# Kernel optimization log

Measured on AMD Instinct MI355X. Metric: run time of the kernel, lower is better.

The kernel has to match this reference:

```python
import jax, jax.numpy as jnp
import numpy as np

# Loihi neuron constants (from a typical slayerSNN network.yaml)
I_DECAY = 1024.0   # current decay (of 4096)
V_DECAY = 128.0    # voltage decay (of 4096)
THETA = 100.0      # firing threshold


def spike_loihi(x):
    """Loihi CUBA neuron dynamics over trailing time axis. x: [..., T] weighted input."""
    xT = jnp.moveaxis(x, -1, 0)  # [T, ...]
    a_i = (4096.0 - I_DECAY) / 4096.0
    a_v = (4096.0 - V_DECAY) / 4096.0

    def step(carry, xt):
        u, v = carry
        u = a_i * u + xt           # synaptic current
        v = a_v * v + u            # membrane voltage
        s = (v >= THETA).astype(x.dtype)
        v = v * (1.0 - s)          # reset on spike
        return (u, v), s

    z = jnp.zeros(xT.shape[1:], x.dtype)
    _, s = jax.lax.scan(step, (z, z), xT)
    return jnp.moveaxis(s, 0, -1)


def delay_shift(x):
    """Shift spikes by 1 timestep along last axis (slayer.delayShift(spike, 1))."""
    return jnp.concatenate([jnp.zeros_like(x[..., :1]), x[..., :-1]], axis=-1)


def conv_t(x, w):
    """Per-timestep 2D conv, padding 1. x: [N,C,H,W,T], w: [O,I,3,3]."""
    N, C, H, W, T = x.shape
    xt = jnp.transpose(x, (0, 4, 1, 2, 3)).reshape(N * T, C, H, W)
    y = jax.lax.conv_general_dilated(xt, w, (1, 1), [(1, 1), (1, 1)],
                                     dimension_numbers=('NCHW', 'OIHW', 'NCHW'))
    O = w.shape[0]
    return jnp.transpose(y.reshape(N, T, O, H, W), (0, 2, 3, 4, 1))


def sum_pool2(x, w):
    """slayer.pool(2): 2x2 sum-pool scaled by (loaded) scalar pool weight."""
    N, C, H, W, T = x.shape
    return x.reshape(N, C, H // 2, 2, W // 2, 2, T).sum(axis=(3, 5)) * w


def setup_inputs() -> dict:
    key = jax.random.key(0)
    ks = jax.random.split(key, 8)
    N, T = 16, 128
    spike = jax.random.bernoulli(ks[0], 0.1, (N, 2, 40, 40, T)).astype(jnp.float32)
    conv1_w = jax.random.normal(ks[1], (8, 2, 3, 3), jnp.float32) * 0.5
    conv2_w = jax.random.normal(ks[2], (16, 8, 3, 3), jnp.float32) * 0.05
    conv3_w = jax.random.normal(ks[3], (32, 16, 3, 3), jnp.float32) * 0.05
    fc1_w = jax.random.normal(ks[4], (512, 10 * 10 * 32), jnp.float32) * 0.02
    pool1_w = jnp.asarray(1.1, jnp.float32)
    pool2_w = jnp.asarray(1.1, jnp.float32)
    return {"spike": spike, "conv1_w": conv1_w, "conv2_w": conv2_w,
            "conv3_w": conv3_w, "pool1_w": pool1_w, "pool2_w": pool2_w,
            "fc1_w": fc1_w}


def reference(spike, conv1_w, conv2_w, conv3_w, pool1_w, pool2_w, fc1_w):
    x = spike_loihi(conv_t(spike, conv1_w * 20.0))    # weightScale=20
    x = delay_shift(x)
    x = spike_loihi(sum_pool2(x, pool1_w))
    x = delay_shift(x)
    x = spike_loihi(conv_t(x, conv2_w * 100.0))       # weightScale=100
    x = delay_shift(x)
    x = spike_loihi(sum_pool2(x, pool2_w))
    x = delay_shift(x)
    x = spike_loihi(conv_t(x, conv3_w * 100.0))       # weightScale=100
    N, T = x.shape[0], x.shape[-1]
    x = x.reshape(N, -1, 1, 1, T)                     # [N, 3200, 1, 1, T]
    x = delay_shift(x)
    x = spike_loihi(jnp.einsum('nchwt,oc->nohwt', x, fc1_w))
    x = delay_shift(x)
    return x
```

## Files before the change

kernel.cpp:

```cpp
#include <hip/hip_runtime.h>
#include <stdint.h>


#define T 128
#define AI 0.75f
#define AV 0.96875f
#define THETA 100.0f

typedef __attribute__((ext_vector_type(8))) short v8s;
typedef __attribute__((ext_vector_type(16))) float v16f;

__device__ __forceinline__ void neuron_step(float x, float& u, float& v, float& s) {
    u = AI * u + x;
    v = AV * v + u;
    s = (v >= THETA) ? 1.0f : 0.0f;
    v = v * (1.0f - s);
}

__global__ __launch_bounds__(256) void conv1_scan(
    const float* __restrict__ in, const float* __restrict__ cw,
    uint8_t* __restrict__ sout)
{
    __shared__ float ldsF[64 * 130];
    int bid = blockIdx.x;
    int wg = bid % 5;
    int hy = (bid / 5) % 40;
    int n  = bid / 200;
    int tid = threadIdx.x;
    int wxl = tid >> 5, tt = tid & 31, t0 = tt * 4;
    int wx = wg * 8 + wxl;

    float4 tap[18];
    #pragma unroll
    for (int c = 0; c < 2; c++)
      #pragma unroll
      for (int dh = 0; dh < 3; dh++)
        #pragma unroll
        for (int dw = 0; dw < 3; dw++) {
            int q = c * 9 + dh * 3 + dw;
            int hh = hy + dh - 1, ww = wx + dw - 1;
            bool ok = (hh >= 0) && (hh < 40) && (ww >= 0) && (ww < 40);
            tap[q] = ok ? *(const float4*)(in +
                (((size_t)(n * 2 + c) * 40 + hh) * 40 + ww) * T + t0)
                        : make_float4(0.f, 0.f, 0.f, 0.f);
        }

    #pragma unroll
    for (int o = 0; o < 8; o++) {
        const float* wp = cw + o * 18;
        float a0 = 0.f, a1 = 0.f, a2 = 0.f, a3 = 0.f;
        #pragma unroll
        for (int q = 0; q < 18; q++) {
            a0 += wp[q] * tap[q].x;  a1 += wp[q] * tap[q].y;
            a2 += wp[q] * tap[q].z;  a3 += wp[q] * tap[q].w;
        }
        float* xr = &ldsF[(o * 8 + wxl) * 130 + t0];
        xr[0] = a0 * 20.0f; xr[1] = a1 * 20.0f;
        xr[2] = a2 * 20.0f; xr[3] = a3 * 20.0f;
    }
    __syncthreads();
    if (tid < 64) {
        int o = tid >> 3, wxl2 = tid & 7;
        float u = 0.f, v = 0.f;
        uint32_t ob[32];
        const float* xr = &ldsF[tid * 130];
        #pragma unroll
        for (int tb = 0; tb < 32; tb++) {
            float s0, s1, s2, s3;
            neuron_step(xr[tb * 4 + 0], u, v, s0);
            neuron_step(xr[tb * 4 + 1], u, v, s1);
            neuron_step(xr[tb * 4 + 2], u, v, s2);
            neuron_step(xr[tb * 4 + 3], u, v, s3);
            ob[tb] = (uint32_t)s0 | ((uint32_t)s1 << 8) |
                     ((uint32_t)s2 << 16) | ((uint32_t)s3 << 24);
        }
        uint32_t* op = (uint32_t*)(sout +
            (((size_t)(n * 8 + o) * 40 + hy) * 40 + wg * 8 + wxl2) * T);
        #pragma unroll
        for (int k = 0; k < 8; k++)
            *(uint4*)&op[k * 4] =
                make_uint4(ob[k*4], ob[k*4+1], ob[k*4+2], ob[k*4+3]);
    }
}

template<int C, int HO, int WO>
__global__ __launch_bounds__(256) void pool_fused(
    const uint8_t* __restrict__ in, const float* __restrict__ pw_ptr,
    uint8_t* __restrict__ out)
{
    __shared__ uint32_t lds[256 * 20];
    int tid = threadIdx.x;
    size_t r0 = (size_t)blockIdx.x * 256;
    float pw = pw_ptr[0];

    float u = 0.f, v = 0.f;
    uint32_t ob[32];
    uint32_t carry = 0;

    #pragma unroll
    for (int tb = 0; tb < 2; tb++) {
        __syncthreads();
        #pragma unroll
        for (int k = 0; k < 4; k++) {
            int f = tid + k * 256;
            int row = f >> 2, q = f & 3;
            int orow = (int)r0 + row;
            int wx = orow % WO;
            int hy = (orow / WO) % HO;
            int c  = (orow / (WO * HO)) % C;
            int nn = orow / (WO * HO * C);
            const uint8_t* p00 = in +
                (((size_t)(nn * C + c) * (2 * HO) + 2 * hy) * (2 * WO) + 2 * wx) * T;
            int off = tb * 64 + q * 16;
            uint4 a = *(const uint4*)(p00 + off);
            uint4 b = *(const uint4*)(p00 + T + off);
            uint4 cc = *(const uint4*)(p00 + 2 * WO * T + off);
            uint4 d = *(const uint4*)(p00 + 2 * WO * T + T + off);
            *(uint4*)&lds[row * 20 + q * 4] =
                make_uint4(a.x + b.x + cc.x + d.x, a.y + b.y + cc.y + d.y,
                           a.z + b.z + cc.z + d.z, a.w + b.w + cc.w + d.w);
        }
        __syncthreads();
        #pragma unroll
        for (int q = 0; q < 4; q++) {
            uint4 w = *(const uint4*)&lds[tid * 20 + q * 4];
            uint32_t words[4] = {w.x, w.y, w.z, w.w};
            #pragma unroll
            for (int j = 0; j < 4; j++) {
                uint32_t cur = words[j];
                uint32_t del = (cur << 8) | carry;
                carry = cur >> 24;
                float s0, s1, s2, s3;
                neuron_step(pw * (float)(del & 0xffu),         u, v, s0);
                neuron_step(pw * (float)((del >> 8) & 0xffu),  u, v, s1);
                neuron_step(pw * (float)((del >> 16) & 0xffu), u, v, s2);
                neuron_step(pw * (float)((del >> 24) & 0xffu), u, v, s3);
                ob[tb * 16 + q * 4 + j] = (uint32_t)s0 | ((uint32_t)s1 << 8) |
                                          ((uint32_t)s2 << 16) | ((uint32_t)s3 << 24);
            }
        }
    }

    uint32_t* op = (uint32_t*)(out + (r0 + tid) * T);
    #pragma unroll
    for (int k = 0; k < 8; k++)
        *(uint4*)&op[k * 4] = make_uint4(ob[k*4], ob[k*4+1], ob[k*4+2], ob[k*4+3]);
}

template<int CIN, int H, int W>
__global__ __launch_bounds__(256) void pad_bf16(
    const uint8_t* __restrict__ s, uint16_t* __restrict__ sP)
{
    int bid = blockIdx.x;
    constexpr int CELLS = (H + 2) * (W + 2);
    int n = bid / CELLS;
    int cell = bid % CELLS;
    int hy = cell / (W + 2) - 1;
    int wx = cell % (W + 2) - 1;
    bool interior = (hy >= 0) && (hy < H) && (wx >= 0) && (wx < W);
    int tid = threadIdx.x;
    int tau = tid >> 1;
    int g = tid & 1;
    uint32_t wb[4] = {0u, 0u, 0u, 0u};
    if (interior && tau >= 1) {
        const uint8_t* sp = s + (((size_t)(n * CIN) * H + hy) * W + wx) * T + tau - 1;
        #pragma unroll
        for (int e = 0; e < 8; e++) {
            int c = g * 8 + e;
            uint32_t b = (c < CIN) ? (uint32_t)sp[(size_t)c * H * W * T] : 0u;
            if (b) wb[e >> 1] |= 0x3F80u << ((e & 1) * 16);
        }
    }
    *(uint4*)(sP + (size_t)bid * 2048 + tau * 16 + g * 8) =
        make_uint4(wb[0], wb[1], wb[2], wb[3]);
}

__global__ __launch_bounds__(64) void apack_w(
    const float* __restrict__ c2w, const float* __restrict__ c3w,
    uint16_t* __restrict__ apk)
{
    int bid = blockIdx.x;
    int conv = bid / 27;
    int plane = (bid % 27) / 9;
    int dlt = bid % 9;
    int lane = threadIdx.x;
    int o = lane & 31, chi = (lane >> 5) * 8;
    int CO = conv ? 32 : 16;
    int CI = conv ? 16 : 8;
    const float* Wp = conv ? c3w : c2w;
    uint32_t wb[4] = {0u, 0u, 0u, 0u};
    #pragma unroll
    for (int e = 0; e < 8; e++) {
        int c = chi + e;
        float w = (o < CO && c < CI) ? Wp[((size_t)o * CI + c) * 9 + dlt] : 0.f;
        uint32_t b0 = __float_as_uint(w);
        uint16_t hi = (uint16_t)(b0 >> 16);
        float r1 = w - __uint_as_float(b0 & 0xFFFF0000u);
        uint32_t b1 = __float_as_uint(r1);
        uint16_t md = (uint16_t)(b1 >> 16);
        float r2 = r1 - __uint_as_float(b1 & 0xFFFF0000u);
        uint16_t lo = (uint16_t)(__float_as_uint(r2) >> 16);
        uint32_t pv = (plane == 0) ? hi : ((plane == 1) ? md : lo);
        wb[e >> 1] |= pv << ((e & 1) * 16);
    }
    *(uint4*)(apk + ((size_t)conv * 27 + plane * 9 + dlt) * 512 + lane * 8) =
        make_uint4(wb[0], wb[1], wb[2], wb[3]);
}

template<int COUT, int PB, int H, int W>
__global__ __launch_bounds__(256, 2) void conv_scan_mfma(
    const uint16_t* __restrict__ sP, const uint16_t* __restrict__ apk,
    float scale, uint8_t* __restrict__ sout)
{
    __shared__ float ldsF[128 * 130];
    constexpr int HW = H * W;
    constexpr int GP = HW / PB;
    int per = (16 * GP) >> 3;
    int vbid = (blockIdx.x & 7) * per + (blockIdx.x >> 3);
    int n = vbid / GP, grp = vbid % GP;
    int tid = threadIdx.x;
    int wv = tid >> 6, lane = tid & 63;
    int l31 = lane & 31, lhi = lane >> 5;
    int t0 = wv * 32;

    const uint16_t* ap = apk + (size_t)lane * 8;
    v8s a0[9], a1[9], a2[9];
    #pragma unroll
    for (int d = 0; d < 9; d++) {
        a0[d] = *(const v8s*)(ap + d * 512);
        a1[d] = *(const v8s*)(ap + (9 + d) * 512);
        a2[d] = *(const v8s*)(ap + (18 + d) * 512);
    }

    #pragma unroll
    for (int p = 0; p < PB; p++) {
        int hw = grp * PB + p;
        int hy = hw / W, wx = hw % W;
        v8s bfr[9];
        #pragma unroll
        for (int d = 0; d < 9; d++) {
            int dh = d / 3, dw = d % 3;
            const uint16_t* src = sP
                + ((size_t)((n * (H + 2) + hy + dh) * (W + 2) + wx + dw)) * 2048
                + (t0 + l31) * 16 + lhi * 8;
            bfr[d] = *(const v8s*)src;
        }
        v16f ac0, ac1, ac2;
        #pragma unroll
        for (int e = 0; e < 16; e++) { ac0[e] = 0.f; ac1[e] = 0.f; ac2[e] = 0.f; }
        #pragma unroll
        for (int d = 0; d < 9; d++) {
            ac0 = __builtin_amdgcn_mfma_f32_32x32x16_bf16(a0[d], bfr[d], ac0, 0, 0, 0);
            ac1 = __builtin_amdgcn_mfma_f32_32x32x16_bf16(a1[d], bfr[d], ac1, 0, 0, 0);
            ac2 = __builtin_amdgcn_mfma_f32_32x32x16_bf16(a2[d], bfr[d], ac2, 0, 0, 0);
        }
        constexpr int NR = (COUT == 32) ? 16 : 8;
        #pragma unroll
        for (int r = 0; r < NR; r++) {
            int o = (r & 3) + 8 * (r >> 2) + 4 * lhi;
            ldsF[(o * PB + p) * 130 + t0 + l31] =
                (ac0[r] + ac1[r] + ac2[r]) * scale;
        }
    }
    __syncthreads();
    if (tid < 128) {
        int o = tid / PB, p = tid % PB;
        int hw = grp * PB + p;
        float u = 0.f, v = 0.f;
        uint32_t ob[32];
        const float* xr = &ldsF[tid * 130];
        #pragma unroll
        for (int tb = 0; tb < 32; tb++) {
            float2 xa = *(const float2*)(xr + tb * 4);
            float2 xb = *(const float2*)(xr + tb * 4 + 2);
            float s0, s1, s2, s3;
            neuron_step(xa.x, u, v, s0); neuron_step(xa.y, u, v, s1);
            neuron_step(xb.x, u, v, s2); neuron_step(xb.y, u, v, s3);
            ob[tb] = (uint32_t)s0 | ((uint32_t)s1 << 8) |
                     ((uint32_t)s2 << 16) | ((uint32_t)s3 << 24);
        }
        uint32_t* op = (uint32_t*)(sout + ((size_t)(n * COUT + o) * HW + hw) * 128);
        #pragma unroll
        for (int k = 0; k < 8; k++)
            *(uint4*)&op[k * 4] =
                make_uint4(ob[k*4], ob[k*4+1], ob[k*4+2], ob[k*4+3]);
    }
}

__global__ __launch_bounds__(256) void wsplit(
    const float* __restrict__ fw, uint16_t* __restrict__ bs)
{
    int i = blockIdx.x * 256 + threadIdx.x;
    float4 wv = *(const float4*)(fw + i * 4);
    float w4[4] = {wv.x, wv.y, wv.z, wv.w};
    uint16_t h[4], m[4], l[4];
    #pragma unroll
    for (int j = 0; j < 4; j++) {
        uint32_t b0 = __float_as_uint(w4[j]);
        h[j] = (uint16_t)(b0 >> 16);
        float r1 = w4[j] - __uint_as_float(b0 & 0xFFFF0000u);
        uint32_t b1 = __float_as_uint(r1);
        m[j] = (uint16_t)(b1 >> 16);
        float r2 = r1 - __uint_as_float(b1 & 0xFFFF0000u);
        l[j] = (uint16_t)(__float_as_uint(r2) >> 16);
    }
    *(ushort4*)(bs +       0 + i * 4) = make_ushort4(h[0], h[1], h[2], h[3]);
    *(ushort4*)(bs + 1638400 + i * 4) = make_ushort4(m[0], m[1], m[2], m[3]);
    *(ushort4*)(bs + 3276800 + i * 4) = make_ushort4(l[0], l[1], l[2], l[3]);
}

__global__ __launch_bounds__(256) void sT_bf16(
    const uint8_t* __restrict__ s5, uint16_t* __restrict__ At)
{
    __shared__ uint8_t tile[64 * 132];
    int bid = blockIdx.x;
    int n = bid / 50;
    int c0 = (bid % 50) * 64;
    int tid = threadIdx.x;
    {
        int row = tid >> 2, q = tid & 3;
        const uint8_t* src = s5 + ((size_t)(n * 3200 + c0 + row)) * T + q * 32;
        *(uint4*)&tile[row * 132 + q * 32]      = *(const uint4*)src;
        *(uint4*)&tile[row * 132 + q * 32 + 16] = *(const uint4*)(src + 16);
    }
    __syncthreads();
    int t = tid >> 1, half = tid & 1;
    uint32_t wb[16];
    if (t == 0) {
        #pragma unroll
        for (int j = 0; j < 16; j++) wb[j] = 0u;
    } else {
        #pragma unroll
        for (int j = 0; j < 16; j++) {
            uint32_t lo = tile[(half * 32 + 2 * j) * 132 + (t - 1)] ? 0x3F80u : 0u;
            uint32_t hi = tile[(half * 32 + 2 * j + 1) * 132 + (t - 1)] ? 0x3F80u : 0u;
            wb[j] = lo | (hi << 16);
        }
    }
    uint16_t* dst = At + ((size_t)(n * 128 + t)) * 3200 + c0 + half * 32;
    #pragma unroll
    for (int k = 0; k < 4; k++)
        *(uint4*)(dst + k * 8) = make_uint4(wb[k*4], wb[k*4+1], wb[k*4+2], wb[k*4+3]);
}

#define GLDS16(g, s) __builtin_amdgcn_global_load_lds( \
    (const __attribute__((address_space(1))) uint32_t*)(g), \
    (__attribute__((address_space(3))) uint32_t*)(s), 16, 0, 0)

__global__ __launch_bounds__(256, 2) void fc_gemm_mfma(
    const uint16_t* __restrict__ At,
    const uint16_t* __restrict__ Bs,
    float* __restrict__ ypart)
{
    __shared__ uint8_t lds[65536];
    int bid = blockIdx.x;
    int n  = bid & 15;
    int ob = (bid >> 4) & 3;
    int ks = bid >> 6;
    int o0 = ob * 128;
    int cbase = ks * 320;

    int tid = threadIdx.x;
    int w4 = tid >> 6;
    int wm = w4 >> 1;
    int wn = w4 & 1;
    int lane = tid & 63;
    int l31 = lane & 31;
    int lhi = lane >> 5;
    int rb = lane >> 3;
    int gsw = (lane & 7) ^ (rb & 7);

    v16f acc[2][2];
    #pragma unroll
    for (int mi = 0; mi < 2; mi++)
        #pragma unroll
        for (int ni = 0; ni < 2; ni++)
            #pragma unroll
            for (int e = 0; e < 16; e++) acc[mi][ni][e] = 0.0f;

    const uint16_t* Abase = At + (size_t)(n * 128) * 3200 + gsw * 8;

    for (int kc = 0; kc < 5; kc++) {
        int c0 = cbase + kc * 64;
        #pragma unroll
        for (int i = 0; i < 4; i++) {
            int cid = i * 4 + w4;
            const uint16_t* src = Abase + (size_t)(cid * 8 + rb) * 3200 + c0;
            GLDS16(src, lds + cid * 1024);
        }
        #pragma unroll
        for (int j = 0; j < 12; j++) {
            int cid = j * 4 + w4;
            int f0 = cid * 1024;
            int s = f0 >> 14;
            int r = ((f0 & 16383) >> 7) + rb;
            const uint16_t* src = Bs + (size_t)(s * 512 + o0 + r) * 3200
                                     + c0 + gsw * 8;
            GLDS16(src, lds + 16384 + f0);
        }
        __syncthreads();
        #pragma unroll
        for (int kf = 0; kf < 4; kf++) {
            int gc = kf * 2 + lhi;
            v8s av[2];
            #pragma unroll
            for (int mi = 0; mi < 2; mi++) {
                int t = wm * 64 + mi * 32 + l31;
                av[mi] = *(const v8s*)(lds + t * 128 + ((gc ^ (t & 7)) << 4));
            }
            #pragma unroll
            for (int s = 0; s < 3; s++) {
                #pragma unroll
                for (int ni = 0; ni < 2; ni++) {
                    int r = wn * 64 + ni * 32 + l31;
                    v8s bv = *(const v8s*)(lds + 16384 + s * 16384 + r * 128
                                           + ((gc ^ (r & 7)) << 4));
                    #pragma unroll
                    for (int mi = 0; mi < 2; mi++)
                        acc[mi][ni] = __builtin_amdgcn_mfma_f32_32x32x16_bf16(
                            av[mi], bv, acc[mi][ni], 0, 0, 0);
                }
            }
        }
        __syncthreads();
    }
    float* yp = ypart + (size_t)ks * 1048576 + (size_t)n * 65536;
    #pragma unroll
    for (int mi = 0; mi < 2; mi++)
        #pragma unroll
        for (int ni = 0; ni < 2; ni++) {
            int o = o0 + wn * 64 + ni * 32 + l31;
            #pragma unroll
            for (int r = 0; r < 16; r++) {
                int trow = wm * 64 + mi * 32 + (r & 3) + 8 * (r >> 2) + 4 * lhi;
                yp[trow * 512 + o] = acc[mi][ni][r];
            }
        }
}

__global__ __launch_bounds__(256) void fc_reduce(
    const float4* __restrict__ yp, float4* __restrict__ ys)
{
    int id = blockIdx.x * 256 + threadIdx.x;
    float4 x = yp[id];
    #pragma unroll
    for (int k = 1; k < 10; k++) {
        float4 y = yp[(size_t)k * 262144 + id];
        x.x += y.x; x.y += y.y; x.z += y.z; x.w += y.w;
    }
    ys[id] = x;
}

__global__ __launch_bounds__(64) void fc_scan(
    const float* __restrict__ ysum,
    float* __restrict__ out)
{
    int id = blockIdx.x * 64 + threadIdx.x;
    int o = id & 511;
    int n = id >> 9;
    float u = 0.f, v = 0.f;
    float prev = 0.f;
    for (int tb = 0; tb < T / 4; tb++) {
        float b0, b1, b2, b3;
        float x, s;
        x = ysum[(n * T + tb * 4 + 0) * 512 + o]; neuron_step(x, u, v, s); b0 = prev; prev = s;
        x = ysum[(n * T + tb * 4 + 1) * 512 + o]; neuron_step(x, u, v, s); b1 = prev; prev = s;
        x = ysum[(n * T + tb * 4 + 2) * 512 + o]; neuron_step(x, u, v, s); b2 = prev; prev = s;
        x = ysum[(n * T + tb * 4 + 3) * 512 + o]; neuron_step(x, u, v, s); b3 = prev; prev = s;
        *(float4*)&out[((size_t)(n * 512 + o)) * T + tb * 4] = make_float4(b0, b1, b2, b3);
    }
}

extern "C" void kernel_launch(void* const* d_in, const int* in_sizes, int n_in,
                              void* d_out, int out_size, void* d_ws, size_t ws_size,
                              hipStream_t stream) {
    const float* spike = (const float*)d_in[0];
    const float* c1w   = (const float*)d_in[1];
    const float* c2w   = (const float*)d_in[2];
    const float* c3w   = (const float*)d_in[3];
    const float* p1w   = (const float*)d_in[4];
    const float* p2w   = (const float*)d_in[5];
    const float* fcw   = (const float*)d_in[6];
    float* out = (float*)d_out;

    char* ws = (char*)d_ws;
    uint8_t*  s1    = (uint8_t*)(ws);
    uint16_t* Bs16  = (uint16_t*)(ws + 26214400);
    uint16_t* Apk   = (uint16_t*)(ws + 36044800);
    uint8_t*  s2    = (uint8_t*)(ws + 36100096);
    uint16_t* s2P   = (uint16_t*)(ws + 42653696);
    uint8_t*  s3    = (uint8_t*)(ws + 74373120);
    uint8_t*  s4    = (uint8_t*)(ws + 87480320);
    uint16_t* s4P   = (uint16_t*)(ws + 90757120);
    uint8_t*  s5    = (uint8_t*)(ws + 100194304);
    uint16_t* At16  = (uint16_t*)(ws + 106747904);
    float*    ypart = (float*)(ws + 119855104);
    float*    ysumb = (float*)(ws + 161798144);

    conv1_scan<<<3200, 256, 0, stream>>>(spike, c1w, s1);
    wsplit<<<1600, 256, 0, stream>>>(fcw, Bs16);
    apack_w<<<54, 64, 0, stream>>>(c2w, c3w, Apk);

    pool_fused<8, 20, 20><<<200, 256, 0, stream>>>(s1, p1w, s2);
    pad_bf16<8, 20, 20><<<16 * 22 * 22, 256, 0, stream>>>(s2, s2P);
    conv_scan_mfma<16, 8, 20, 20><<<800, 256, 0, stream>>>(s2P, Apk, 100.0f, s3);

    pool_fused<16, 10, 10><<<100, 256, 0, stream>>>(s3, p2w, s4);
    pad_bf16<16, 10, 10><<<16 * 12 * 12, 256, 0, stream>>>(s4, s4P);
    conv_scan_mfma<32, 4, 10, 10><<<400, 256, 0, stream>>>(s4P, Apk + 13824, 100.0f, s5);

    sT_bf16<<<800, 256, 0, stream>>>(s5, At16);
    fc_gemm_mfma<<<640, 256, 0, stream>>>(At16, Bs16, ypart);
    fc_reduce<<<1024, 256, 0, stream>>>((const float4*)ypart, (float4*)ysumb);
    fc_scan<<<128, 64, 0, stream>>>(ysumb, out);
}
```

Measured before the change: 255.8 us.

## Fuse pool scan with bf16 halo-padded packing and remap block order

```diff
diff --git a/kernel.cpp b/kernel.cpp
--- a/kernel.cpp
+++ b/kernel.cpp
@@ -22,7 +22,8 @@
     uint8_t* __restrict__ sout)
 {
     __shared__ float ldsF[64 * 130];
-    int bid = blockIdx.x;
+    int bid0 = blockIdx.x;
+    int bid = (bid0 & 7) * 400 + (bid0 >> 3);
     int wg = bid % 5;
     int hy = (bid / 5) % 40;
     int n  = bid / 200;
@@ -84,13 +85,19 @@
 }
 
 template<int C, int HO, int WO>
-__global__ __launch_bounds__(256) void pool_fused(
+__global__ __launch_bounds__(320) void pool_pad(
     const uint8_t* __restrict__ in, const float* __restrict__ pw_ptr,
-    uint8_t* __restrict__ out)
-{
-    __shared__ uint32_t lds[256 * 20];
+    uint16_t* __restrict__ sP)
+{
+    constexpr int CB = 320 / C;
+    constexpr int GP = (HO * WO) / CB;
+    __shared__ uint8_t raw[320 * 132];
+    uint32_t* ldsF = (uint32_t*)raw;
+    uint8_t*  sbuf = raw;
+
+    int bid = blockIdx.x;
+    int grp = bid % GP, n = bid / GP;
     int tid = threadIdx.x;
-    size_t r0 = (size_t)blockIdx.x * 256;
     float pw = pw_ptr[0];
 
     float u = 0.f, v = 0.f;
@@ -102,28 +109,26 @@
         __syncthreads();
         #pragma unroll
         for (int k = 0; k < 4; k++) {
-            int f = tid + k * 256;
+            int f = tid + k * 320;
             int row = f >> 2, q = f & 3;
-            int orow = (int)r0 + row;
-            int wx = orow % WO;
-            int hy = (orow / WO) % HO;
-            int c  = (orow / (WO * HO)) % C;
-            int nn = orow / (WO * HO * C);
+            int c = row / CB, p = row % CB;
+            int hw = grp * CB + p;
+            int wx = hw % WO, hy = hw / WO;
             const uint8_t* p00 = in +
-                (((size_t)(nn * C + c) * (2 * HO) + 2 * hy) * (2 * WO) + 2 * wx) * T;
+                (((size_t)(n * C + c) * (2 * HO) + 2 * hy) * (2 * WO) + 2 * wx) * T;
             int off = tb * 64 + q * 16;
             uint4 a = *(const uint4*)(p00 + off);
             uint4 b = *(const uint4*)(p00 + T + off);
             uint4 cc = *(const uint4*)(p00 + 2 * WO * T + off);
             uint4 d = *(const uint4*)(p00 + 2 * WO * T + T + off);
-            *(uint4*)&lds[row * 20 + q * 4] =
+            *(uint4*)&ldsF[row * 20 + q * 4] =
                 make_uint4(a.x + b.x + cc.x + d.x, a.y + b.y + cc.y + d.y,
                            a.z + b.z + cc.z + d.z, a.w + b.w + cc.w + d.w);
         }
         __syncthreads();
         #pragma unroll
         for (int q = 0; q < 4; q++) {
-            uint4 w = *(const uint4*)&lds[tid * 20 + q * 4];
+            uint4 w = *(const uint4*)&ldsF[tid * 20 + q * 4];
             uint32_t words[4] = {w.x, w.y, w.z, w.w};
             #pragma unroll
             for (int j = 0; j < 4; j++) {
@@ -141,38 +146,46 @@
         }
     }
 
-    uint32_t* op = (uint32_t*)(out + (r0 + tid) * T);
-    #pragma unroll
-    for (int k = 0; k < 8; k++)
-        *(uint4*)&op[k * 4] = make_uint4(ob[k*4], ob[k*4+1], ob[k*4+2], ob[k*4+3]);
-}
-
-template<int CIN, int H, int W>
-__global__ __launch_bounds__(256) void pad_bf16(
-    const uint8_t* __restrict__ s, uint16_t* __restrict__ sP)
-{
+    __syncthreads();
+    #pragma unroll
+    for (int j = 0; j < 32; j++)
+        *(uint32_t*)&sbuf[tid * 132 + j * 4] = ob[j];
+    __syncthreads();
+
+    constexpr int CHK = CB * 128;
+    #pragma unroll
+    for (int k = 0; k < CHK / 320; k++) {
+        int ci = k * 320 + tid;
+        int p = ci >> 7, tau = ci & 127;
+        int hw = grp * CB + p;
+        int wx = hw % WO, hy = hw / WO;
+        uint32_t wb[8];
+        #pragma unroll
+        for (int e = 0; e < 16; e += 2) {
+            uint32_t lo = 0u, hi = 0u;
+            if (tau >= 1) {
+                if (e < C)     lo = sbuf[(e * CB + p) * 132 + tau - 1] ? 0x3F80u : 0u;
+                if (e + 1 < C) hi = sbuf[((e + 1) * CB + p) * 132 + tau - 1] ? 0x3F80u : 0u;
+            }
+            wb[e >> 1] = lo | (hi << 16);
+        }
+        uint16_t* dst = sP + ((size_t)((n * (HO + 2) + hy + 1) * (WO + 2)
+                                       + wx + 1)) * 2048 + tau * 16;
+        *(uint4*)dst       = make_uint4(wb[0], wb[1], wb[2], wb[3]);
+        *(uint4*)(dst + 8) = make_uint4(wb[4], wb[5], wb[6], wb[7]);
+    }
+}
+
+template<int H, int W>
+__global__ __launch_bounds__(256) void zero_halo(uint16_t* __restrict__ sP)
+{
+    constexpr int CELLS = (H + 2) * (W + 2);
     int bid = blockIdx.x;
-    constexpr int CELLS = (H + 2) * (W + 2);
-    int n = bid / CELLS;
     int cell = bid % CELLS;
-    int hy = cell / (W + 2) - 1;
-    int wx = cell % (W + 2) - 1;
-    bool interior = (hy >= 0) && (hy < H) && (wx >= 0) && (wx < W);
-    int tid = threadIdx.x;
-    int tau = tid >> 1;
-    int g = tid & 1;
-    uint32_t wb[4] = {0u, 0u, 0u, 0u};
-    if (interior && tau >= 1) {
-        const uint8_t* sp = s + (((size_t)(n * CIN) * H + hy) * W + wx) * T + tau - 1;
-        #pragma unroll
-        for (int e = 0; e < 8; e++) {
-            int c = g * 8 + e;
-            uint32_t b = (c < CIN) ? (uint32_t)sp[(size_t)c * H * W * T] : 0u;
-            if (b) wb[e >> 1] |= 0x3F80u << ((e & 1) * 16);
-        }
-    }
-    *(uint4*)(sP + (size_t)bid * 2048 + tau * 16 + g * 8) =
-        make_uint4(wb[0], wb[1], wb[2], wb[3]);
+    int hy = cell / (W + 2), wx = cell % (W + 2);
+    if (hy >= 1 && hy <= H && wx >= 1 && wx <= W) return;
+    *(uint4*)((uint8_t*)sP + (size_t)bid * 4096 + threadIdx.x * 16) =
+        make_uint4(0u, 0u, 0u, 0u);
 }
 
 __global__ __launch_bounds__(64) void apack_w(
@@ -353,7 +366,8 @@
     float* __restrict__ ypart)
 {
     __shared__ uint8_t lds[65536];
-    int bid = blockIdx.x;
+    int bid0 = blockIdx.x;
+    int bid = (bid0 & 7) * 80 + (bid0 >> 3);
     int n  = bid & 15;
     int ob = (bid >> 4) & 3;
     int ks = bid >> 6;
@@ -487,26 +501,24 @@
     uint8_t*  s1    = (uint8_t*)(ws);
     uint16_t* Bs16  = (uint16_t*)(ws + 26214400);
     uint16_t* Apk   = (uint16_t*)(ws + 36044800);
-    uint8_t*  s2    = (uint8_t*)(ws + 36100096);
-    uint16_t* s2P   = (uint16_t*)(ws + 42653696);
-    uint8_t*  s3    = (uint8_t*)(ws + 74373120);
-    uint8_t*  s4    = (uint8_t*)(ws + 87480320);
-    uint16_t* s4P   = (uint16_t*)(ws + 90757120);
-    uint8_t*  s5    = (uint8_t*)(ws + 100194304);
-    uint16_t* At16  = (uint16_t*)(ws + 106747904);
-    float*    ypart = (float*)(ws + 119855104);
-    float*    ysumb = (float*)(ws + 161798144);
+    uint16_t* s2P   = (uint16_t*)(ws + 36100096);
+    uint8_t*  s3    = (uint8_t*)(ws + 67819520);
+    uint16_t* s4P   = (uint16_t*)(ws + 80926720);
+    uint8_t*  s5    = (uint8_t*)(ws + 90363904);
+    uint16_t* At16  = (uint16_t*)(ws + 96917504);
+    float*    ypart = (float*)(ws + 110024704);
+    float*    ysumb = (float*)(ws + 151967744);
 
     conv1_scan<<<3200, 256, 0, stream>>>(spike, c1w, s1);
     wsplit<<<1600, 256, 0, stream>>>(fcw, Bs16);
     apack_w<<<54, 64, 0, stream>>>(c2w, c3w, Apk);
-
-    pool_fused<8, 20, 20><<<200, 256, 0, stream>>>(s1, p1w, s2);
-    pad_bf16<8, 20, 20><<<16 * 22 * 22, 256, 0, stream>>>(s2, s2P);
+    zero_halo<20, 20><<<16 * 484, 256, 0, stream>>>(s2P);
+    zero_halo<10, 10><<<16 * 144, 256, 0, stream>>>(s4P);
+
+    pool_pad<8, 20, 20><<<160, 320, 0, stream>>>(s1, p1w, s2P);
     conv_scan_mfma<16, 8, 20, 20><<<800, 256, 0, stream>>>(s2P, Apk, 100.0f, s3);
 
-    pool_fused<16, 10, 10><<<100, 256, 0, stream>>>(s3, p2w, s4);
-    pad_bf16<16, 10, 10><<<16 * 12 * 12, 256, 0, stream>>>(s4, s4P);
+    pool_pad<16, 10, 10><<<80, 320, 0, stream>>>(s3, p2w, s4P);
     conv_scan_mfma<32, 4, 10, 10><<<400, 256, 0, stream>>>(s4P, Apk + 13824, 100.0f, s5);
 
     sT_bf16<<<800, 256, 0, stream>>>(s5, At16);
```

Result: no change. 259.0 us (+1.2%).
